# Optimization experiments

Measured on AMD Instinct MI355X. Metric: run time of the kernel, lower is better.

Reference implementation:

```python
import jax, jax.numpy as jnp
import numpy as np

H = 4          # num_heads
MB = 4         # ttt mini_batch_size
GRP = 4        # scan_checkpoint_group_size
TTT_LR = 0.1   # ttt_base_lr
ERF_C = 0.7071067811865476   # 1/sqrt(2)
PDF_C = 0.3989422804014327   # 1/sqrt(2*pi)


def _gelu(z):
    return 0.5 * z * (1.0 + jax.scipy.special.erf(z * ERF_C))


def _gelu_grad(z):
    return 0.5 * (1.0 + jax.scipy.special.erf(z * ERF_C)) + z * jnp.exp(-0.5 * z * z) * PDF_C


def _ln(x, w, b, eps):
    mu = x.mean(-1, keepdims=True)
    var = ((x - mu) ** 2).mean(-1, keepdims=True)
    return w * (x - mu) / jnp.sqrt(var + eps) + b


def _ln_l2_bwd(z, w, b, target, eps=1e-6):
    # grad of 0.5*||LN(z; w, b) - target||^2 w.r.t. z (fused LN backward)
    mu = z.mean(-1, keepdims=True)
    var = ((z - mu) ** 2).mean(-1, keepdims=True)
    std = jnp.sqrt(var + eps)
    zhat = (z - mu) / std
    y = w * zhat + b
    g = w * (y - target)
    return (g - g.mean(-1, keepdims=True) - zhat * (g * zhat).mean(-1, keepdims=True)) / std


def _conv1d(x, w, b, pad):
    # x: [B, Cin, L], w: [Cout, Cin, K]
    y = jax.lax.conv_general_dilated(x, w, (1,), [(pad, pad)], dimension_numbers=("NCH", "OIH", "NCH"))
    return y + b[None, :, None]


def _ttt(x, wq, wk, wv, wo, W1, b1, W2, b2, lnw, lnb):
    # x: [B, L, D];  ttt_mlp fast-weight scan over mini-batches of size MB
    B, L, D = x.shape
    d = D // H
    nmb = L // MB
    ng = nmb // GRP

    def split(w):
        # [B,L,D] -> [ng, GRP, B, H, MB, d]
        return (x @ w).reshape(B, L, H, d).transpose(0, 2, 1, 3).reshape(B, H, ng, GRP, MB, d).transpose(2, 3, 0, 1, 4, 5)

    XQ, XK, XV = split(wq), split(wk), split(wv)
    lw = lnw[None, :, None, :]  # [1,H,1,d]
    lb = lnb[None, :, None, :]
    eta = TTT_LR / MB

    carry = (jnp.broadcast_to(W1, (B, H, d, 4 * d)),
             jnp.broadcast_to(b1, (B, H, 1, 4 * d)),
             jnp.broadcast_to(W2, (B, H, 4 * d, d)),
             jnp.broadcast_to(b2, (B, H, 1, d)))

    def step(c, inp):
        W1c, b1c, W2c, b2c = c
        xq, xk, xv = inp  # each [B,H,MB,d]
        Z1 = jnp.einsum('bhmd,bhdk->bhmk', xk, W1c) + b1c
        X2 = _gelu(Z1)
        Z2 = jnp.einsum('bhmk,bhkd->bhmd', X2, W2c) + b2c
        gZ2 = _ln_l2_bwd(Z2, lw, lb, xv - xk)
        gZ1 = jnp.einsum('bhmd,bhkd->bhmk', gZ2, W2c) * _gelu_grad(Z1)
        W1n = W1c - eta * jnp.einsum('bhmd,bhmk->bhdk', xk, gZ1)
        b1n = b1c - eta * gZ1.sum(2, keepdims=True)
        W2n = W2c - eta * jnp.einsum('bhmk,bhmd->bhkd', X2, gZ2)
        b2n = b2c - eta * gZ2.sum(2, keepdims=True)
        Z1q = jnp.einsum('bhmd,bhdk->bhmk', xq, W1n) + b1n
        Z2q = jnp.einsum('bhmk,bhkd->bhmd', _gelu(Z1q), W2n) + b2n
        return (W1n, b1n, W2n, b2n), xq + _ln(Z2q, lw, lb, 1e-6)

    @jax.checkpoint
    def group(c, inp_g):
        return jax.lax.scan(step, c, inp_g)

    _, out = jax.lax.scan(group, carry, (XQ, XK, XV))  # [ng,GRP,B,H,MB,d]
    out = out.transpose(2, 3, 0, 1, 4, 5).reshape(B, H, L, d).transpose(0, 2, 1, 3).reshape(B, L, D)
    return x + out @ wo


def reference(x, conv1_w, conv1_b, convs_w, convs_b, ln_w, ln_b, wq, wk, wv, wo,
              ttt_W1, ttt_b1, ttt_W2, ttt_b2, ttt_ln_w, ttt_ln_b,
              fc_w, fc_b, fc2_w, fc2_b, fc3_w, fc3_b):
    h = x.transpose(0, 2, 1)                       # [B, dim1, L]
    h = jax.nn.relu(_conv1d(h, conv1_w, conv1_b, 0))
    acts = []
    for i in range(8):
        h = jax.nn.relu(_conv1d(h, convs_w[i], convs_b[i], 1))
        acts.append(h)
    h = acts[1] + acts[3] + acts[5] + acts[7]      # x2 + x4 + x6 + x8
    h = h.transpose(0, 2, 1)                       # [B, L, dim3]
    h = _ln(h, ln_w, ln_b, 1e-5)
    h = _ttt(h, wq, wk, wv, wo, ttt_W1, ttt_b1, ttt_W2, ttt_b2, ttt_ln_w, ttt_ln_b)
    h = _ln(h, ln_w, ln_b, 1e-5)                   # module reuses self.layer_norm
    h = h @ fc_w + fc_b
    h = h @ fc2_w + fc2_b
    return h @ fc3_w + fc3_b                       # [B, L, 1]


def setup_inputs() -> dict:
    key = jax.random.key(0)
    ks = jax.random.split(key, 12)
    B, L, dim1, dim2, dim3 = 4, 1024, 64, 512, 256
    Hn, dh = 4, 64

    def n(k, shape):
        return jax.random.normal(k, shape, jnp.float32) * 0.02

    return {
        "x": jax.random.normal(ks[0], (B, L, dim1), jnp.float32),
        "conv1_w": n(ks[1], (dim3, dim1, 1)),
        "conv1_b": jnp.zeros((dim3,), jnp.float32),
        "convs_w": n(ks[2], (8, dim3, dim3, 3)),
        "convs_b": jnp.zeros((8, dim3), jnp.float32),
        "ln_w": jnp.ones((dim3,), jnp.float32),
        "ln_b": jnp.zeros((dim3,), jnp.float32),
        "wq": n(ks[3], (dim3, dim3)),
        "wk": n(ks[4], (dim3, dim3)),
        "wv": n(ks[5], (dim3, dim3)),
        "wo": n(ks[6], (dim3, dim3)),
        "ttt_W1": n(ks[7], (Hn, dh, 4 * dh)),
        "ttt_b1": jnp.zeros((Hn, 1, 4 * dh), jnp.float32),
        "ttt_W2": n(ks[8], (Hn, 4 * dh, dh)),
        "ttt_b2": jnp.zeros((Hn, 1, dh), jnp.float32),
        "ttt_ln_w": jnp.ones((Hn, dh), jnp.float32),
        "ttt_ln_b": jnp.zeros((Hn, dh), jnp.float32),
        "fc_w": n(ks[9], (dim3, dim2)),
        "fc_b": jnp.zeros((dim2,), jnp.float32),
        "fc2_w": n(ks[10], (dim2, dim1)),
        "fc2_b": jnp.zeros((dim1,), jnp.float32),
        "fc3_w": n(ks[11], (dim1, 1)),
        "fc3_b": jnp.zeros((1,), jnp.float32),
    }
```

## Files before the change

### kernel.cpp

```cpp
#include <hip/hip_runtime.h>
#include <hip/hip_bf16.h>


#define ERF_CF 0.70710678118654752f
#define PDF_CF 0.3989422804014327f
#define ETA 0.025f

typedef __attribute__((ext_vector_type(8))) short bfrag;
typedef __attribute__((ext_vector_type(4))) float f32x4;

union FB { bfrag v; unsigned short u[8]; unsigned d[4]; };

__device__ __forceinline__ float wsum(float v) {
#pragma unroll
  for (int o = 32; o > 0; o >>= 1) v += __shfl_xor(v, o, 64);
  return v;
}

__device__ __forceinline__ unsigned pack_split(float x) {
  unsigned u = __float_as_uint(x);
  unsigned hb = u & 0xFFFF0000u;
  float lf = x - __uint_as_float(hb);
  return hb | (__float_as_uint(lf) >> 16);
}
// ... 52 lines not shown
    val = fc2w[in * 64 + out];
  }
  unsigned short hs, ls;
  split2(val, hs, ls);
  WH[id] = hs;
  WL[id] = ls;
}

__global__ __launch_bounds__(256) void zero_halo_pl(
    unsigned short* __restrict__ cAH, unsigned short* __restrict__ cAL,
    unsigned short* __restrict__ cBH, unsigned short* __restrict__ cBL) {
  int id = blockIdx.x * 256 + threadIdx.x;
  int buf = id >> 11;
  int r = id & 2047;
  int b = r >> 9, row = (r >> 8) & 1, c = r & 255;
  unsigned short* p = buf == 0 ? cAH : buf == 1 ? cAL : buf == 2 ? cBH : cBL;
  p[(b * 1026 + row * 1025) * 256 + c] = 0;
}

template <int AF32, int HALOA, int BIAS, int RELU, int EPI, int ACC>
__global__ __launch_bounds__(256) void gemm_mf(
    const unsigned short* __restrict__ AH, const unsigned short* __restrict__ AL,
    const float* __restrict__ Af32,
    const unsigned short* __restrict__ BH, const unsigned short* __restrict__ BL,
    const float* __restrict__ bias,
    const unsigned short* __restrict__ resH, const unsigned short* __restrict__ resL,
    float* __restrict__ outF, unsigned short* __restrict__ outH,
    unsigned short* __restrict__ outL, float* __restrict__ acc4,
    int N, int K) {
  const int tid = threadIdx.x;
  const int w = tid >> 6, lane = tid & 63;
  const int a = lane & 15, g = lane >> 4;
  const int s = w >> 1, ch = w & 1;
  const int bm = blockIdx.x * 32, bn = blockIdx.y * 64;
  const int rowA = bm + 16 * s + a;
  long abase;
  if constexpr (HALOA)
    abase = (long)((rowA >> 10) * 1026 + (rowA & 1023)) * 256;
  else
    abase = (long)rowA * K;
  const int cb0 = bn + (ch * 2) * 16 + a;
  const int cb1 = cb0 + 16;
  f32x4 acc0 = {0.f, 0.f, 0.f, 0.f}, acc1 = {0.f, 0.f, 0.f, 0.f};
#pragma unroll 2
  for (int kk = 0; kk < K; kk += 32) {
    FB ah, al;
    if constexpr (AF32) {
      const float* ap = Af32 + abase + kk + g * 8;
      float av[8];
      *(float4*)&av[0] = *(const float4*)ap;
      *(float4*)&av[4] = *(const float4*)(ap + 4);
#pragma unroll
      for (int e = 0; e < 8; ++e) split2(av[e], ah.u[e], al.u[e]);
    } else {
      ah.v = *(const bfrag*)&AH[abase + kk + g * 8];
      al.v = *(const bfrag*)&AL[abase + kk + g * 8];
    }
    FB b0h, b0l, b1h, b1l;
    b0h.v = *(const bfrag*)&BH[(long)cb0 * K + kk + g * 8];
    b0l.v = *(const bfrag*)&BL[(long)cb0 * K + kk + g * 8];
    b1h.v = *(const bfrag*)&BH[(long)cb1 * K + kk + g * 8];
    b1l.v = *(const bfrag*)&BL[(long)cb1 * K + kk + g * 8];
    acc0 = mm3(ah.v, al.v, b0h.v, b0l.v, acc0);
    acc1 = mm3(ah.v, al.v, b1h.v, b1l.v, acc1);
  }
#pragma unroll
  for (int i = 0; i < 2; ++i) {
    f32x4 av = i ? acc1 : acc0;
    int col = i ? cb1 : cb0;
    float bv = 0.f;
    if constexpr (BIAS) bv = bias[col];
#pragma unroll
    for (int q = 0; q < 4; ++q) {
      int r = bm + 16 * s + g * 4 + q;
      float val = av[q] + bv;
      if constexpr (RELU) val = fmaxf(val, 0.f);
      if constexpr (EPI == 4) {
        long ri = (long)r * N + col;
        val += uns(resH[ri], resL[ri]);
      }
      if constexpr (EPI == 0 || EPI == 4) {
        outF[(long)r * N + col] = val;
      } else if constexpr (EPI == 1) {
        long hi = (long)((r >> 10) * 1026 + (r & 1023) + 1) * 256 + col;
        unsigned short hs, ls;
        split2(val, hs, ls);
        outH[hi] = hs;
        outL[hi] = ls;
      } else if constexpr (EPI == 2) {
        int b_ = r >> 10, l = r & 1023, hq = col >> 6;
        long oidx = (((long)(b_ * 4 + hq) * 1024 + l) << 6) + (col & 63);
        outF[oidx] = val;
      } else if constexpr (EPI == 3) {
        long oi = (long)r * N + col;
        unsigned short hs, ls;
        split2(val, hs, ls);
        outH[oi] = hs;
        outL[oi] = ls;
      }
      if constexpr (ACC == 1) {
        acc4[(long)r * 256 + col] = val;
      } else if constexpr (ACC == 2) {
        acc4[(long)r * 256 + col] += val;
      }
    }
  }
}

__global__ __launch_bounds__(256) void ln_pl(const float* __restrict__ in,
                                             unsigned short* __restrict__ oH,
                                             unsigned short* __restrict__ oL,
                                             const float* __restrict__ w,
                                             const float* __restrict__ bb,
                                             float eps) {
  int row = blockIdx.x * 4 + (threadIdx.x >> 6);
  int l = threadIdx.x & 63;
  float4 v = ((const float4*)(in + (long)row * 256))[l];
  float s = wsum(v.x + v.y + v.z + v.w);
  float mu = s * (1.0f / 256.0f);
  float dx = v.x - mu, dy = v.y - mu, dz = v.z - mu, dw = v.w - mu;
  float rstd = rsqrtf(wsum(dx * dx + dy * dy + dz * dz + dw * dw) * (1.0f / 256.0f) + eps);
  float4 wv = ((const float4*)w)[l];
  float4 bv = ((const float4*)bb)[l];
  float rr[4];
  rr[0] = wv.x * dx * rstd + bv.x;
  rr[1] = wv.y * dy * rstd + bv.y;
  rr[2] = wv.z * dz * rstd + bv.z;
  rr[3] = wv.w * dw * rstd + bv.w;
  long base = (long)row * 256 + l * 4;
#pragma unroll
  for (int j = 0; j < 4; ++j) {
    unsigned short hs, ls;
    split2(rr[j], hs, ls);
    oH[base + j] = hs;
    oL[base + j] = ls;
  }
}

__global__ __launch_bounds__(512, 2) void ttt_mfma(
    const float* __restrict__ XQ, const float* __restrict__ XK,
    const float* __restrict__ XV, const float* __restrict__ W1i,
    const float* __restrict__ B1i, const float* __restrict__ W2i,
    const float* __restrict__ B2i, const float* __restrict__ LNW,
    const float* __restrict__ LNB, unsigned short* __restrict__ outH,
    unsigned short* __restrict__ outL) {
  extern __shared__ char smem[];
  unsigned short* W2Hp  = (unsigned short*)smem;
  unsigned short* W2Lp  = W2Hp + 256 * 72;
  unsigned short* W2THp = W2Lp + 256 * 72;
  unsigned short* W2TLp = W2THp + 64 * 264;
  unsigned short* X2Hp  = W2TLp + 64 * 264;
  unsigned short* X2Lp  = X2Hp + 4 * 272;
  unsigned short* xkHp  = X2Lp + 4 * 272;
  unsigned short* xkLp  = xkHp + 4 * 80;
  unsigned short* xqHp  = xkLp + 4 * 80;
  unsigned short* xqLp  = xqHp + 4 * 80;
  unsigned short* gZHp  = xqLp + 4 * 80;
  unsigned short* gZLp  = gZHp + 4 * 80;
  float* X2F  = (float*)(gZLp + 4 * 80);
  float* gZ1f = X2F + 4 * 264;
  float* Z2f  = gZ1f + 1024;
  float* redS = Z2f + 256;
  float* xvL  = redS + 512;
  float* b2L  = xvL + 256;
  float* lwL  = b2L + 64;
  float* lbL  = lwL + 64;

  const int bh = blockIdx.x, b = bh >> 2, h = bh & 3;
  const int t = threadIdx.x;
  const int w8 = t >> 6;
  const int lane = t & 63;
  const int a = lane & 15, g = lane >> 4;
  const bool rowv = (a < 4), g0 = (g == 0);
  const int c0 = 32 * w8 + a;
  const int c1 = 32 * w8 + 16 + a;
  const int kh = w8 & 1;
  const int jc = (w8 >> 1) * 16 + a;

  FB zf; zf.d[0] = zf.d[1] = zf.d[2] = zf.d[3] = 0;

  FB w1h[2][2], w1l[2][2];
#pragma unroll
  for (int i = 0; i < 2; ++i) {
    int cc = 32 * w8 + i * 16 + a;
#pragma unroll
    for (int kc = 0; kc < 2; ++kc) {
#pragma unroll
      for (int e = 0; e < 8; ++e) {
        int k = kc * 32 + g * 8 + e;
        unsigned p = pack_split(W1i[(h * 64 + k) * 256 + cc]);
        w1h[i][kc].u[e] = (unsigned short)(p >> 16);
        w1l[i][kc].u[e] = (unsigned short)(p & 0xFFFFu);
      }
    }
  }
  float b1r0 = B1i[h * 256 + c0];
  float b1r1 = B1i[h * 256 + c1];

  for (int i = 0; i < 32; ++i) {
    int id = t + i * 512;
    int k = id >> 6, j = id & 63;
    unsigned p = pack_split(W2i[(h * 256 + k) * 64 + j]);
    W2Hp[k * 72 + j] = (unsigned short)(p >> 16);
    W2Lp[k * 72 + j] = (unsigned short)(p & 0xFFFFu);
    int j2 = id >> 8, k2 = id & 255;
    unsigned q = pack_split(W2i[(h * 256 + k2) * 64 + j2]);
    W2THp[j2 * 264 + k2] = (unsigned short)(q >> 16);
    W2TLp[j2 * 264 + k2] = (unsigned short)(q & 0xFFFFu);
  }
  if (t < 64) { b2L[t] = B2i[h * 64 + t]; lwL[t] = LNW[h * 64 + t]; lbL[t] = LNB[h * 64 + t]; }

  const long chain = (long)bh * 65536;
  float rk = 0.f, rv = 0.f, rq = 0.f;
  if (t >= 256) {
    int u = t - 256;
    rk = XK[chain + u]; rv = XV[chain + u]; rq = XQ[chain + u];
  }

  for (int n = 0; n < 256; ++n) {
    if (t >= 256) {
      int u = t - 256, m = u >> 6, k = u & 63;
      unsigned short hs, ls;
      split2(rk, hs, ls); xkHp[m * 80 + k] = hs; xkLp[m * 80 + k] = ls;
      split2(rq, hs, ls); xqHp[m * 80 + k] = hs; xqLp[m * 80 + k] = ls;
      xvL[u] = rv;
    }
    __syncthreads();

    float gpA[4] = {0.f, 0.f, 0.f, 0.f}, gpB[4] = {0.f, 0.f, 0.f, 0.f};

    {
      f32x4 A0 = (f32x4){b1r0, b1r0, b1r0, b1r0};
      f32x4 A1 = (f32x4){b1r1, b1r1, b1r1, b1r1};
#pragma unroll
      for (int kc = 0; kc < 2; ++kc) {
        int base = kc * 32 + g * 8;
        FB ah = zf, al = zf;
        if (rowv) {
          ah.v = *(const bfrag*)&xkHp[a * 80 + base];
          al.v = *(const bfrag*)&xkLp[a * 80 + base];
        }
        A0 = mm3(ah.v, al.v, w1h[0][kc].v, w1l[0][kc].v, A0);
        A1 = mm3(ah.v, al.v, w1h[1][kc].v, w1l[1][kc].v, A1);
      }
      if (g0) {
#pragma unroll
        for (int q = 0; q < 4; ++q) {
          float z = A0[q];
          float er = erff(z * ERF_CF);
          float hh = 0.5f * (1.0f + er);
          float x2 = z * hh;
          gpA[q] = hh + z * __expf(-0.5f * z * z) * PDF_CF;
          unsigned short hs, ls;
          split2(x2, hs, ls);
          X2Hp[q * 272 + c0] = hs; X2Lp[q * 272 + c0] = ls;
          X2F[q * 264 + c0] = x2;
          z = A1[q];
          er = erff(z * ERF_CF);
          hh = 0.5f * (1.0f + er);
          x2 = z * hh;
          gpB[q] = hh + z * __expf(-0.5f * z * z) * PDF_CF;
          split2(x2, hs, ls);
          X2Hp[q * 272 + c1] = hs; X2Lp[q * 272 + c1] = ls;
          X2F[q * 264 + c1] = x2;
        }
      }
    }
    __syncthreads();

    {
      f32x4 acc = (f32x4){0.f, 0.f, 0.f, 0.f};
#pragma unroll
      for (int k4 = 0; k4 < 4; ++k4) {
        int base = (kh * 4 + k4) * 32 + g * 8;
        FB ah = zf, al = zf, bhf, blf;
        if (rowv) {
          ah.v = *(const bfrag*)&X2Hp[a * 272 + base];
          al.v = *(const bfrag*)&X2Lp[a * 272 + base];
        }
        bhf.v = *(const bfrag*)&W2THp[jc * 264 + base];
        blf.v = *(const bfrag*)&W2TLp[jc * 264 + base];
        acc = mm3(ah.v, al.v, bhf.v, blf.v, acc);
      }
      if (g0) {
#pragma unroll
        for (int q = 0; q < 4; ++q) redS[(kh * 4 + q) * 64 + jc] = acc[q];
      }
    }
    __syncthreads();

    if (t < 256) {
      int m = w8, j = lane;
      float z2 = b2L[j] + redS[m * 64 + j] + redS[256 + m * 64 + j];
      float mu = wsum(z2) * (1.0f / 64.0f);
      float dv = z2 - mu;
      float var = wsum(dv * dv) * (1.0f / 64.0f);
      float stdv = sqrtf(var + 1e-6f);
      float zh = dv / stdv;
      float lw = lwL[j], lb = lbL[j];
      float xkf = uns(xkHp[m * 80 + j], xkLp[m * 80 + j]);
      float tgt = xvL[m * 64 + j] - xkf;
      float gg = lw * (lw * zh + lb - tgt);
      float gs = wsum(gg) * (1.0f / 64.0f);
      float gzs = wsum(gg * zh) * (1.0f / 64.0f);
      float gz2 = (gg - gs - zh * gzs) / stdv;
      unsigned short hs, ls;
      split2(gz2, hs, ls);
      gZHp[m * 80 + j] = hs; gZLp[m * 80 + j] = ls;
      Z2f[m * 64 + j] = gz2;
    } else if (n + 1 < 256) {
      int u = t - 256;
      long nb = chain + (long)(n + 1) * 256;
      rk = XK[nb + u]; rv = XV[nb + u]; rq = XQ[nb + u];
    }
    __syncthreads();

    {
      f32x4 A0 = (f32x4){0.f, 0.f, 0.f, 0.f};
      f32x4 A1 = (f32x4){0.f, 0.f, 0.f, 0.f};
#pragma unroll
      for (int kc = 0; kc < 2; ++kc) {
        int base = kc * 32 + g * 8;
        FB ah = zf, al = zf, b0h, b0l, b1h, b1l;
        if (rowv) {
          ah.v = *(const bfrag*)&gZHp[a * 80 + base];
          al.v = *(const bfrag*)&gZLp[a * 80 + base];
        }
        b0h.v = *(const bfrag*)&W2Hp[c0 * 72 + base];
        b0l.v = *(const bfrag*)&W2Lp[c0 * 72 + base];
        b1h.v = *(const bfrag*)&W2Hp[c1 * 72 + base];
        b1l.v = *(const bfrag*)&W2Lp[c1 * 72 + base];
        A0 = mm3(ah.v, al.v, b0h.v, b0l.v, A0);
        A1 = mm3(ah.v, al.v, b1h.v, b1l.v, A1);
      }
      if (g0) {
#pragma unroll
        for (int q = 0; q < 4; ++q) {
          gZ1f[q * 256 + c0] = A0[q] * gpA[q];
          gZ1f[q * 256 + c1] = A1[q] * gpB[q];
        }
      }
      {
        int jr = t & 63, kb = (t >> 6) * 32;
        float gz0 = Z2f[jr], gz1 = Z2f[64 + jr], gz2 = Z2f[128 + jr], gz3 = Z2f[192 + jr];
#pragma unroll
        for (int kk = 0; kk < 32; kk += 8) {
          int kb8 = kb + kk;
          float x0[8], x1[8], x2[8], x3[8];
          *(float4*)&x0[0] = *(const float4*)&X2F[kb8];        *(float4*)&x0[4] = *(const float4*)&X2F[kb8 + 4];
          *(float4*)&x1[0] = *(const float4*)&X2F[264 + kb8];  *(float4*)&x1[4] = *(const float4*)&X2F[264 + kb8 + 4];
          *(float4*)&x2[0] = *(const float4*)&X2F[528 + kb8];  *(float4*)&x2[4] = *(const float4*)&X2F[528 + kb8 + 4];
          *(float4*)&x3[0] = *(const float4*)&X2F[792 + kb8];  *(float4*)&x3[4] = *(const float4*)&X2F[792 + kb8 + 4];
          FB oh, ol, nh, nl;
          oh.v = *(const bfrag*)&W2THp[jr * 264 + kb8];
          ol.v = *(const bfrag*)&W2TLp[jr * 264 + kb8];
#pragma unroll
          for (int e = 0; e < 8; ++e) {
            float uu = fmaf(x3[e], gz3, fmaf(x2[e], gz2, fmaf(x1[e], gz1, x0[e] * gz0)));
            float f = fmaf(-ETA, uu, fb_el(oh, ol, e));
            unsigned short hs, ls;
            split2(f, hs, ls);
            nh.u[e] = hs; nl.u[e] = ls;
          }
          *(bfrag*)&W2THp[jr * 264 + kb8] = nh.v;
          *(bfrag*)&W2TLp[jr * 264 + kb8] = nl.v;
        }
      }
    }
    __syncthreads();

    {
      float gzA0 = gZ1f[c0], gzA1 = gZ1f[256 + c0], gzA2 = gZ1f[512 + c0], gzA3 = gZ1f[768 + c0];
      float gzB0 = gZ1f[c1], gzB1 = gZ1f[256 + c1], gzB2 = gZ1f[512 + c1], gzB3 = gZ1f[768 + c1];
      b1r0 = fmaf(-ETA, ((gzA0 + gzA1) + gzA2) + gzA3, b1r0);
      b1r1 = fmaf(-ETA, ((gzB0 + gzB1) + gzB2) + gzB3, b1r1);
#pragma unroll
      for (int kc = 0; kc < 2; ++kc) {
        int base = kc * 32 + g * 8;
        FB x0h, x0l, x1h, x1l, x2h, x2l, x3h, x3l;
        x0h.v = *(const bfrag*)&xkHp[base];       x0l.v = *(const bfrag*)&xkLp[base];
        x1h.v = *(const bfrag*)&xkHp[80 + base];  x1l.v = *(const bfrag*)&xkLp[80 + base];
        x2h.v = *(const bfrag*)&xkHp[160 + base]; x2l.v = *(const bfrag*)&xkLp[160 + base];
        x3h.v = *(const bfrag*)&xkHp[240 + base]; x3l.v = *(const bfrag*)&xkLp[240 + base];
#pragma unroll
        for (int e = 0; e < 8; ++e) {
          float k0 = fb_el(x0h, x0l, e), k1 = fb_el(x1h, x1l, e);
          float k2 = fb_el(x2h, x2l, e), k3 = fb_el(x3h, x3l, e);
          float uA = fmaf(k3, gzA3, fmaf(k2, gzA2, fmaf(k1, gzA1, k0 * gzA0)));
          float uB = fmaf(k3, gzB3, fmaf(k2, gzB2, fmaf(k1, gzB1, k0 * gzB0)));
          float fA = fmaf(-ETA, uA, fb_el(w1h[0][kc], w1l[0][kc], e));
          float fB = fmaf(-ETA, uB, fb_el(w1h[1][kc], w1l[1][kc], e));
          unsigned short hs, ls;
          split2(fA, hs, ls); w1h[0][kc].u[e] = hs; w1l[0][kc].u[e] = ls;
          split2(fB, hs, ls); w1h[1][kc].u[e] = hs; w1l[1][kc].u[e] = ls;
        }
      }
      {
        f32x4 A0 = (f32x4){b1r0, b1r0, b1r0, b1r0};
        f32x4 A1 = (f32x4){b1r1, b1r1, b1r1, b1r1};
#pragma unroll
        for (int kc = 0; kc < 2; ++kc) {
          int base = kc * 32 + g * 8;
          FB ah = zf, al = zf;
          if (rowv) {
            ah.v = *(const bfrag*)&xqHp[a * 80 + base];
            al.v = *(const bfrag*)&xqLp[a * 80 + base];
          }
          A0 = mm3(ah.v, al.v, w1h[0][kc].v, w1l[0][kc].v, A0);
          A1 = mm3(ah.v, al.v, w1h[1][kc].v, w1l[1][kc].v, A1);
        }
        if (g0) {
#pragma unroll
          for (int q = 0; q < 4; ++q) {
            float z = A0[q];
            float x2 = 0.5f * z * (1.0f + erff(z * ERF_CF));
            unsigned short hs, ls;
            split2(x2, hs, ls);
            X2Hp[q * 272 + c0] = hs; X2Lp[q * 272 + c0] = ls;
            z = A1[q];
            x2 = 0.5f * z * (1.0f + erff(z * ERF_CF));
            split2(x2, hs, ls);
            X2Hp[q * 272 + c1] = hs; X2Lp[q * 272 + c1] = ls;
          }
        }
      }
      {
        int kr = t & 255, jh = (t >> 8) * 32;
        float xk0 = X2F[kr], xk1 = X2F[264 + kr], xk2 = X2F[528 + kr], xk3 = X2F[792 + kr];
#pragma unroll
        for (int jj = 0; jj < 32; jj += 8) {
          int jb = jh + jj;
          float g0f[8], g1f[8], g2f[8], g3f[8];
          *(float4*)&g0f[0] = *(const float4*)&Z2f[jb];        *(float4*)&g0f[4] = *(const float4*)&Z2f[jb + 4];
          *(float4*)&g1f[0] = *(const float4*)&Z2f[64 + jb];   *(float4*)&g1f[4] = *(const float4*)&Z2f[64 + jb + 4];
          *(float4*)&g2f[0] = *(const float4*)&Z2f[128 + jb];  *(float4*)&g2f[4] = *(const float4*)&Z2f[128 + jb + 4];
          *(float4*)&g3f[0] = *(const float4*)&Z2f[192 + jb];  *(float4*)&g3f[4] = *(const float4*)&Z2f[192 + jb + 4];
          FB oh, ol, nh, nl;
          oh.v = *(const bfrag*)&W2Hp[kr * 72 + jb];
          ol.v = *(const bfrag*)&W2Lp[kr * 72 + jb];
#pragma unroll
          for (int e = 0; e < 8; ++e) {
            float uu = fmaf(xk3, g3f[e], fmaf(xk2, g2f[e], fmaf(xk1, g1f[e], xk0 * g0f[e])));
            float f = fmaf(-ETA, uu, fb_el(oh, ol, e));
            unsigned short hs, ls;
            split2(f, hs, ls);
            nh.u[e] = hs; nl.u[e] = ls;
          }
          *(bfrag*)&W2Hp[kr * 72 + jb] = nh.v;
          *(bfrag*)&W2Lp[kr * 72 + jb] = nl.v;
        }
      }
      if (t < 64)
        b2L[t] -= ETA * (((Z2f[t] + Z2f[64 + t]) + Z2f[128 + t]) + Z2f[192 + t]);
    }
    __syncthreads();

    {
      f32x4 acc = (f32x4){0.f, 0.f, 0.f, 0.f};
#pragma unroll
      for (int k4 = 0; k4 < 4; ++k4) {
        int base = (kh * 4 + k4) * 32 + g * 8;
        FB ah = zf, al = zf, bhf, blf;
        if (rowv) {
          ah.v = *(const bfrag*)&X2Hp[a * 272 + base];
          al.v = *(const bfrag*)&X2Lp[a * 272 + base];
        }
        bhf.v = *(const bfrag*)&W2THp[jc * 264 + base];
        blf.v = *(const bfrag*)&W2TLp[jc * 264 + base];
        acc = mm3(ah.v, al.v, bhf.v, blf.v, acc);
      }
      if (g0) {
#pragma unroll
        for (int q = 0; q < 4; ++q) redS[(kh * 4 + q) * 64 + jc] = acc[q];
      }
    }
    __syncthreads();

    if (t < 256) {
      int m = w8, j = lane;
      float z = b2L[j] + redS[m * 64 + j] + redS[256 + m * 64 + j];
      float mu = wsum(z) * (1.0f / 64.0f);
      float dv = z - mu;
      float var = wsum(dv * dv) * (1.0f / 64.0f);
      float rstd = rsqrtf(var + 1e-6f);
      float xqf = uns(xqHp[m * 80 + j], xqLp[m * 80 + j]);
      float val = lwL[j] * dv * rstd + lbL[j] + xqf;
      long oidx = ((long)(b * 1024 + n * 4 + m)) * 256 + h * 64 + j;
      unsigned short hs, ls;
      split2(val, hs, ls);
      outH[oidx] = hs;
      outL[oidx] = ls;
    }
    __syncthreads();
  }
}

__global__ __launch_bounds__(256) void fc3_kernel(const float* __restrict__ f2,
                                                  const float* __restrict__ w,
                                                  const float* __restrict__ bias,
                                                  float* __restrict__ o) {
  int m = blockIdx.x * 4 + (threadIdx.x >> 6);
  int lane = threadIdx.x & 63;
  float v = f2[m * 64 + lane] * w[lane];
  v = wsum(v);
  if (lane == 0) o[m] = v + bias[0];
}

extern "C" void kernel_launch(void* const* d_in, const int* in_sizes, int n_in,
                              void* d_out, int out_size, void* d_ws, size_t ws_size,
                              hipStream_t stream) {
  const float* x       = (const float*)d_in[0];
  const float* conv1_w = (const float*)d_in[1];
  const float* conv1_b = (const float*)d_in[2];
  const float* convs_w = (const float*)d_in[3];
  const float* convs_b = (const float*)d_in[4];
  const float* ln_w    = (const float*)d_in[5];
  const float* ln_b    = (const float*)d_in[6];
  const float* wq      = (const float*)d_in[7];
  const float* wk      = (const float*)d_in[8];
  const float* wv      = (const float*)d_in[9];
  const float* wo      = (const float*)d_in[10];
  const float* ttt_W1  = (const float*)d_in[11];
  const float* ttt_b1  = (const float*)d_in[12];
  const float* ttt_W2  = (const float*)d_in[13];
  const float* ttt_b2  = (const float*)d_in[14];
  const float* ttt_lnw = (const float*)d_in[15];
  const float* ttt_lnb = (const float*)d_in[16];
  const float* fc_w    = (const float*)d_in[17];
  const float* fc_b    = (const float*)d_in[18];
  const float* fc2_w   = (const float*)d_in[19];
  const float* fc2_b   = (const float*)d_in[20];
  const float* fc3_w   = (const float*)d_in[21];
  const float* fc3_b   = (const float*)d_in[22];

  unsigned short* U = (unsigned short*)d_ws;
  unsigned short* WH   = U;
  unsigned short* WL   = U + 2015232;
  unsigned short* cAH  = U + 4030464;
  unsigned short* cAL  = U + 5081088;
  unsigned short* cBH  = U + 6131712;
  unsigned short* cBL  = U + 7182336;
  unsigned short* tlnH = U + 8232960;
  unsigned short* tlnL = U + 9281536;
  unsigned short* toH  = U + 10330112;
  unsigned short* toL  = U + 11378688;
  float* F = (float*)d_ws;
  float* sum4 = F + 6213632;
  float* XQ   = sum4;
  float* tfull = sum4;
  float* XK   = F + 7262208;
  float* XV   = F + 8310784;
  unsigned short* f1H = (unsigned short*)XK;
  unsigned short* f1L = (unsigned short*)XV;
  float* f2 = (float*)toH;
  unsigned short* h2H = cAH;
  unsigned short* h2L = cAL;

  const int W_WT1 = 0, W_WT = 16384, W_QKVO = 1589248, W_FC = 1851392, W_FC2 = 1982464;

  dim3 blk(256);

  zero_halo_pl<<<32, blk, 0, stream>>>(cAH, cAL, cBH, cBL);
  prep_all<<<7872, blk, 0, stream>>>(conv1_w, convs_w, wq, wk, wv, wo, fc_w,
                                     fc2_w, WH, WL);

  gemm_mf<1, 0, 1, 1, 1, 0><<<dim3(128, 4), blk, 0, stream>>>(
      nullptr, nullptr, x, WH + W_WT1, WL + W_WT1, conv1_b, nullptr, nullptr,
      nullptr, cAH, cAL, nullptr, 256, 64);

  for (int i = 0; i < 8; ++i) {
    const unsigned short* iH = (i % 2 == 0) ? cAH : cBH;
    const unsigned short* iL = (i % 2 == 0) ? cAL : cBL;
    unsigned short* oH = (i % 2 == 0) ? cBH : cAH;
    unsigned short* oL = (i % 2 == 0) ? cBL : cAL;
    const unsigned short* bH = WH + W_WT + i * 196608;
    const unsigned short* bL = WL + W_WT + i * 196608;
    const float* bp = convs_b + i * 256;
    if (i == 1)
      gemm_mf<0, 1, 1, 1, 1, 1><<<dim3(128, 4), blk, 0, stream>>>(
          iH, iL, nullptr, bH, bL, bp, nullptr, nullptr, nullptr, oH, oL, sum4,
          256, 768);
    else if (i == 3 || i == 5 || i == 7)
      gemm_mf<0, 1, 1, 1, 1, 2><<<dim3(128, 4), blk, 0, stream>>>(
          iH, iL, nullptr, bH, bL, bp, nullptr, nullptr, nullptr, oH, oL, sum4,
          256, 768);
    else
      gemm_mf<0, 1, 1, 1, 1, 0><<<dim3(128, 4), blk, 0, stream>>>(
          iH, iL, nullptr, bH, bL, bp, nullptr, nullptr, nullptr, oH, oL,
          nullptr, 256, 768);
  }

  ln_pl<<<1024, blk, 0, stream>>>(sum4, tlnH, tlnL, ln_w, ln_b, 1e-5f);

  gemm_mf<0, 0, 0, 0, 2, 0><<<dim3(128, 4), blk, 0, stream>>>(
      tlnH, tlnL, nullptr, WH + W_QKVO + 0 * 65536, WL + W_QKVO + 0 * 65536,
      nullptr, nullptr, nullptr, XQ, nullptr, nullptr, nullptr, 256, 256);
  gemm_mf<0, 0, 0, 0, 2, 0><<<dim3(128, 4), blk, 0, stream>>>(
      tlnH, tlnL, nullptr, WH + W_QKVO + 1 * 65536, WL + W_QKVO + 1 * 65536,
      nullptr, nullptr, nullptr, XK, nullptr, nullptr, nullptr, 256, 256);
  gemm_mf<0, 0, 0, 0, 2, 0><<<dim3(128, 4), blk, 0, stream>>>(
      tlnH, tlnL, nullptr, WH + W_QKVO + 2 * 65536, WL + W_QKVO + 2 * 65536,
      nullptr, nullptr, nullptr, XV, nullptr, nullptr, nullptr, 256, 256);

  const int TTT_LDS = 162688;
  (void)hipFuncSetAttribute((const void*)ttt_mfma,
                            hipFuncAttributeMaxDynamicSharedMemorySize, TTT_LDS);
  ttt_mfma<<<16, dim3(512), TTT_LDS, stream>>>(XQ, XK, XV, ttt_W1, ttt_b1,
                                               ttt_W2, ttt_b2, ttt_lnw, ttt_lnb,
                                               toH, toL);

  gemm_mf<0, 0, 0, 0, 4, 0><<<dim3(128, 4), blk, 0, stream>>>(
      toH, toL, nullptr, WH + W_QKVO + 3 * 65536, WL + W_QKVO + 3 * 65536,
      nullptr, tlnH, tlnL, tfull, nullptr, nullptr, nullptr, 256, 256);

  ln_pl<<<1024, blk, 0, stream>>>(tfull, h2H, h2L, ln_w, ln_b, 1e-5f);

  gemm_mf<0, 0, 1, 0, 3, 0><<<dim3(128, 8), blk, 0, stream>>>(
      h2H, h2L, nullptr, WH + W_FC, WL + W_FC, fc_b, nullptr, nullptr, nullptr,
      f1H, f1L, nullptr, 512, 256);
  gemm_mf<0, 0, 1, 0, 0, 0><<<dim3(128, 1), blk, 0, stream>>>(
      f1H, f1L, nullptr, WH + W_FC2, WL + W_FC2, fc2_b, nullptr, nullptr, f2,
      nullptr, nullptr, nullptr, 64, 512);
  fc3_kernel<<<1024, blk, 0, stream>>>(f2, fc3_w, fc3_b, (float*)d_out);
}
```

Before: 2.931 ms.

## Compute TTT query outputs with Gram-matrix correction instead of post-update matmuls

Before the weights are updated, the query projection through the old W1 is computed together with the key projection. The post-update Z1 and Z2 for the queries are then built algebraically from Gram terms (xq·xk and X2q·X2k) and the gradients. This removes the dependence of the output stage on the updated W1 and W2 and cuts one barrier per mini-batch from the sequential scan. The cost is extra MFMA work, extra shuffle reductions, and possible numeric differences from reassociating the terms.

```diff
diff --git a/kernel.cpp b/kernel.cpp
--- a/kernel.cpp
+++ b/kernel.cpp
@@ -241,6 +241,8 @@
   float* b2L  = xvL + 256;
   float* lwL  = b2L + 64;
   float* lbL  = lwL + 64;
+  float* G1L  = lbL + 64;
+  float* G2L  = G1L + 16;
 
   const int bh = blockIdx.x, b = bh >> 2, h = bh & 3;
   const int t = threadIdx.x;
@@ -252,6 +254,9 @@
   const int c1 = 32 * w8 + 16 + a;
   const int kh = w8 & 1;
   const int jc = (w8 >> 1) * 16 + a;
+  const int gp_ = 2 * w8 + (lane >> 5);
+  const int gmq = gp_ >> 2, gmk = gp_ & 3;
+  const int gr = lane & 31;
 
   FB zf; zf.d[0] = zf.d[1] = zf.d[2] = zf.d[3] = 0;
 
@@ -308,16 +313,22 @@
     {
       f32x4 A0 = (f32x4){b1r0, b1r0, b1r0, b1r0};
       f32x4 A1 = (f32x4){b1r1, b1r1, b1r1, b1r1};
+      f32x4 Q0 = (f32x4){b1r0, b1r0, b1r0, b1r0};
+      f32x4 Q1 = (f32x4){b1r1, b1r1, b1r1, b1r1};
 #pragma unroll
       for (int kc = 0; kc < 2; ++kc) {
         int base = kc * 32 + g * 8;
-        FB ah = zf, al = zf;
+        FB kh_ = zf, kl_ = zf, qh_ = zf, ql_ = zf;
         if (rowv) {
-          ah.v = *(const bfrag*)&xkHp[a * 80 + base];
-          al.v = *(const bfrag*)&xkLp[a * 80 + base];
-        }
-        A0 = mm3(ah.v, al.v, w1h[0][kc].v, w1l[0][kc].v, A0);
-        A1 = mm3(ah.v, al.v, w1h[1][kc].v, w1l[1][kc].v, A1);
+          kh_.v = *(const bfrag*)&xkHp[a * 80 + base];
+          kl_.v = *(const bfrag*)&xkLp[a * 80 + base];
+          qh_.v = *(const bfrag*)&xqHp[a * 80 + base];
+          ql_.v = *(const bfrag*)&xqLp[a * 80 + base];
+        }
+        A0 = mm3(kh_.v, kl_.v, w1h[0][kc].v, w1l[0][kc].v, A0);
+        A1 = mm3(kh_.v, kl_.v, w1h[1][kc].v, w1l[1][kc].v, A1);
+        Q0 = mm3(qh_.v, ql_.v, w1h[0][kc].v, w1l[0][kc].v, Q0);
+        Q1 = mm3(qh_.v, ql_.v, w1h[1][kc].v, w1l[1][kc].v, Q1);
       }
       if (g0) {
 #pragma unroll
@@ -339,6 +350,8 @@
           split2(x2, hs, ls);
           X2Hp[q * 272 + c1] = hs; X2Lp[q * 272 + c1] = ls;
           X2F[q * 264 + c1] = x2;
+          gZ1f[q * 256 + c0] = Q0[q];
+          gZ1f[q * 256 + c1] = Q1[q];
         }
       }
     }
@@ -362,6 +375,16 @@
 #pragma unroll
         for (int q = 0; q < 4; ++q) redS[(kh * 4 + q) * 64 + jc] = acc[q];
       }
+      float s = uns(xqHp[gmq * 80 + gr], xqLp[gmq * 80 + gr]) *
+                    uns(xkHp[gmk * 80 + gr], xkLp[gmk * 80 + gr]) +
+                uns(xqHp[gmq * 80 + gr + 32], xqLp[gmq * 80 + gr + 32]) *
+                    uns(xkHp[gmk * 80 + gr + 32], xkLp[gmk * 80 + gr + 32]);
+      s += __shfl_xor(s, 16, 64);
+      s += __shfl_xor(s, 8, 64);
+      s += __shfl_xor(s, 4, 64);
+      s += __shfl_xor(s, 2, 64);
+      s += __shfl_xor(s, 1, 64);
+      if (gr == 0) G1L[gp_] = s;
     }
     __syncthreads();
 
@@ -410,12 +433,144 @@
         A1 = mm3(ah.v, al.v, b1h.v, b1l.v, A1);
       }
       if (g0) {
+        float gzc0[4], gzc1[4], q0v[4], q1v[4];
 #pragma unroll
         for (int q = 0; q < 4; ++q) {
-          gZ1f[q * 256 + c0] = A0[q] * gpA[q];
-          gZ1f[q * 256 + c1] = A1[q] * gpB[q];
-        }
-      }
+          gzc0[q] = A0[q] * gpA[q];
+          gzc1[q] = A1[q] * gpB[q];
+          q0v[q] = gZ1f[q * 256 + c0];
+          q1v[q] = gZ1f[q * 256 + c1];
+        }
+#pragma unroll
+        for (int q = 0; q < 4; ++q) {
+          float d0 = G1L[q * 4 + 0] + 1.0f, d1 = G1L[q * 4 + 1] + 1.0f;
+          float d2 = G1L[q * 4 + 2] + 1.0f, d3 = G1L[q * 4 + 3] + 1.0f;
+          float corr0 = fmaf(d3, gzc0[3], fmaf(d2, gzc0[2], fmaf(d1, gzc0[1], d0 * gzc0[0])));
+          float corr1 = fmaf(d3, gzc1[3], fmaf(d2, gzc1[2], fmaf(d1, gzc1[1], d0 * gzc1[0])));
+          float z0 = fmaf(-ETA, corr0, q0v[q]);
+          float z1 = fmaf(-ETA, corr1, q1v[q]);
+          float x20 = 0.5f * z0 * (1.0f + erff(z0 * ERF_CF));
+          float x21 = 0.5f * z1 * (1.0f + erff(z1 * ERF_CF));
+          unsigned short hs, ls;
+          split2(x20, hs, ls);
+          X2Hp[q * 272 + c0] = hs; X2Lp[q * 272 + c0] = ls;
+          split2(x21, hs, ls);
+          X2Hp[q * 272 + c1] = hs; X2Lp[q * 272 + c1] = ls;
+          gZ1f[q * 256 + c0] = gzc0[q];
+          gZ1f[q * 256 + c1] = gzc1[q];
+        }
+      }
+    }
+    __syncthreads();
+
+    float b2r = 0.f;
+    {
+      f32x4 acc = (f32x4){0.f, 0.f, 0.f, 0.f};
+#pragma unroll
+      for (int k4 = 0; k4 < 4; ++k4) {
+        int base = (kh * 4 + k4) * 32 + g * 8;
+        FB ah = zf, al = zf, bhf, blf;
+        if (rowv) {
+          ah.v = *(const bfrag*)&X2Hp[a * 272 + base];
+          al.v = *(const bfrag*)&X2Lp[a * 272 + base];
+        }
+        bhf.v = *(const bfrag*)&W2THp[jc * 264 + base];
+        blf.v = *(const bfrag*)&W2TLp[jc * 264 + base];
+        acc = mm3(ah.v, al.v, bhf.v, blf.v, acc);
+      }
+      if (g0) {
+#pragma unroll
+        for (int q = 0; q < 4; ++q) redS[(kh * 4 + q) * 64 + jc] = acc[q];
+      }
+      float s = 0.f;
+#pragma unroll
+      for (int kk = 0; kk < 256; kk += 32)
+        s = fmaf(uns(X2Hp[gmq * 272 + kk + gr], X2Lp[gmq * 272 + kk + gr]),
+                 X2F[gmk * 264 + kk + gr], s);
+      s += __shfl_xor(s, 16, 64);
+      s += __shfl_xor(s, 8, 64);
+      s += __shfl_xor(s, 4, 64);
+      s += __shfl_xor(s, 2, 64);
+      s += __shfl_xor(s, 1, 64);
+      if (gr == 0) G2L[gp_] = s;
+      float gzA0 = gZ1f[c0], gzA1 = gZ1f[256 + c0], gzA2 = gZ1f[512 + c0], gzA3 = gZ1f[768 + c0];
+      float gzB0 = gZ1f[c1], gzB1 = gZ1f[256 + c1], gzB2 = gZ1f[512 + c1], gzB3 = gZ1f[768 + c1];
+      b1r0 = fmaf(-ETA, ((gzA0 + gzA1) + gzA2) + gzA3, b1r0);
+      b1r1 = fmaf(-ETA, ((gzB0 + gzB1) + gzB2) + gzB3, b1r1);
+#pragma unroll
+      for (int kc = 0; kc < 2; ++kc) {
+        int base = kc * 32 + g * 8;
+        FB x0h, x0l, x1h, x1l, x2h, x2l, x3h, x3l;
+        x0h.v = *(const bfrag*)&xkHp[base];       x0l.v = *(const bfrag*)&xkLp[base];
+        x1h.v = *(const bfrag*)&xkHp[80 + base];  x1l.v = *(const bfrag*)&xkLp[80 + base];
+        x2h.v = *(const bfrag*)&xkHp[160 + base]; x2l.v = *(const bfrag*)&xkLp[160 + base];
+        x3h.v = *(const bfrag*)&xkHp[240 + base]; x3l.v = *(const bfrag*)&xkLp[240 + base];
+#pragma unroll
+        for (int e = 0; e < 8; ++e) {
+          float k0 = fb_el(x0h, x0l, e), k1 = fb_el(x1h, x1l, e);
+          float k2 = fb_el(x2h, x2l, e), k3 = fb_el(x3h, x3l, e);
+          float uA = fmaf(k3, gzA3, fmaf(k2, gzA2, fmaf(k1, gzA1, k0 * gzA0)));
+          float uB = fmaf(k3, gzB3, fmaf(k2, gzB2, fmaf(k1, gzB1, k0 * gzB0)));
+          float fA = fmaf(-ETA, uA, fb_el(w1h[0][kc], w1l[0][kc], e));
+          float fB = fmaf(-ETA, uB, fb_el(w1h[1][kc], w1l[1][kc], e));
+          unsigned short hs, ls;
+          split2(fA, hs, ls); w1h[0][kc].u[e] = hs; w1l[0][kc].u[e] = ls;
+          split2(fB, hs, ls); w1h[1][kc].u[e] = hs; w1l[1][kc].u[e] = ls;
+        }
+      }
+      {
+        int kr = t & 255, jh = (t >> 8) * 32;
+        float xk0 = X2F[kr], xk1 = X2F[264 + kr], xk2 = X2F[528 + kr], xk3 = X2F[792 + kr];
+#pragma unroll
+        for (int jj = 0; jj < 32; jj += 8) {
+          int jb = jh + jj;
+          float g0f[8], g1f[8], g2f[8], g3f[8];
+          *(float4*)&g0f[0] = *(const float4*)&Z2f[jb];        *(float4*)&g0f[4] = *(const float4*)&Z2f[jb + 4];
+          *(float4*)&g1f[0] = *(const float4*)&Z2f[64 + jb];   *(float4*)&g1f[4] = *(const float4*)&Z2f[64 + jb + 4];
+          *(float4*)&g2f[0] = *(const float4*)&Z2f[128 + jb];  *(float4*)&g2f[4] = *(const float4*)&Z2f[128 + jb + 4];
+          *(float4*)&g3f[0] = *(const float4*)&Z2f[192 + jb];  *(float4*)&g3f[4] = *(const float4*)&Z2f[192 + jb + 4];
+          FB oh, ol, nh, nl;
+          oh.v = *(const bfrag*)&W2Hp[kr * 72 + jb];
+          ol.v = *(const bfrag*)&W2Lp[kr * 72 + jb];
+#pragma unroll
+          for (int e = 0; e < 8; ++e) {
+            float uu = fmaf(xk3, g3f[e], fmaf(xk2, g2f[e], fmaf(xk1, g1f[e], xk0 * g0f[e])));
+            float f = fmaf(-ETA, uu, fb_el(oh, ol, e));
+            unsigned short hs, ls;
+            split2(f, hs, ls);
+            nh.u[e] = hs; nl.u[e] = ls;
+          }
+          *(bfrag*)&W2Hp[kr * 72 + jb] = nh.v;
+          *(bfrag*)&W2Lp[kr * 72 + jb] = nl.v;
+        }
+      }
+      if (t < 256) b2r = b2L[lane];
+    }
+    __syncthreads();
+
+    {
+      if (t < 256) {
+        int m = w8, j = lane;
+        float z = b2r + redS[m * 64 + j] + redS[256 + m * 64 + j];
+        float corr = fmaf(G2L[m * 4 + 0] + 1.f, Z2f[j],
+                     fmaf(G2L[m * 4 + 1] + 1.f, Z2f[64 + j],
+                     fmaf(G2L[m * 4 + 2] + 1.f, Z2f[128 + j],
+                          (G2L[m * 4 + 3] + 1.f) * Z2f[192 + j])));
+        z = fmaf(-ETA, corr, z);
+        float mu = wsum(z) * (1.0f / 64.0f);
+        float dv = z - mu;
+        float var = wsum(dv * dv) * (1.0f / 64.0f);
+        float rstd = rsqrtf(var + 1e-6f);
+        float xqf = uns(xqHp[m * 80 + j], xqLp[m * 80 + j]);
+        float val = lwL[j] * dv * rstd + lbL[j] + xqf;
+        long oidx = ((long)(b * 1024 + n * 4 + m)) * 256 + h * 64 + j;
+        unsigned short hs, ls;
+        split2(val, hs, ls);
+        outH[oidx] = hs;
+        outL[oidx] = ls;
+      }
+      if (t < 64)
+        b2L[t] -= ETA * (((Z2f[t] + Z2f[64 + t]) + Z2f[128 + t]) + Z2f[192 + t]);
       {
         int jr = t & 63, kb = (t >> 6) * 32;
         float gz0 = Z2f[jr], gz1 = Z2f[64 + jr], gz2 = Z2f[128 + jr], gz3 = Z2f[192 + jr];
@@ -442,130 +597,6 @@
           *(bfrag*)&W2TLp[jr * 264 + kb8] = nl.v;
         }
       }
-    }
-    __syncthreads();
-
-    {
-      float gzA0 = gZ1f[c0], gzA1 = gZ1f[256 + c0], gzA2 = gZ1f[512 + c0], gzA3 = gZ1f[768 + c0];
-      float gzB0 = gZ1f[c1], gzB1 = gZ1f[256 + c1], gzB2 = gZ1f[512 + c1], gzB3 = gZ1f[768 + c1];
-      b1r0 = fmaf(-ETA, ((gzA0 + gzA1) + gzA2) + gzA3, b1r0);
-      b1r1 = fmaf(-ETA, ((gzB0 + gzB1) + gzB2) + gzB3, b1r1);
-#pragma unroll
-      for (int kc = 0; kc < 2; ++kc) {
-        int base = kc * 32 + g * 8;
-        FB x0h, x0l, x1h, x1l, x2h, x2l, x3h, x3l;
-        x0h.v = *(const bfrag*)&xkHp[base];       x0l.v = *(const bfrag*)&xkLp[base];
-        x1h.v = *(const bfrag*)&xkHp[80 + base];  x1l.v = *(const bfrag*)&xkLp[80 + base];
-        x2h.v = *(const bfrag*)&xkHp[160 + base]; x2l.v = *(const bfrag*)&xkLp[160 + base];
-        x3h.v = *(const bfrag*)&xkHp[240 + base]; x3l.v = *(const bfrag*)&xkLp[240 + base];
-#pragma unroll
-        for (int e = 0; e < 8; ++e) {
-          float k0 = fb_el(x0h, x0l, e), k1 = fb_el(x1h, x1l, e);
-          float k2 = fb_el(x2h, x2l, e), k3 = fb_el(x3h, x3l, e);
-          float uA = fmaf(k3, gzA3, fmaf(k2, gzA2, fmaf(k1, gzA1, k0 * gzA0)));
-          float uB = fmaf(k3, gzB3, fmaf(k2, gzB2, fmaf(k1, gzB1, k0 * gzB0)));
-          float fA = fmaf(-ETA, uA, fb_el(w1h[0][kc], w1l[0][kc], e));
-          float fB = fmaf(-ETA, uB, fb_el(w1h[1][kc], w1l[1][kc], e));
-          unsigned short hs, ls;
-          split2(fA, hs, ls); w1h[0][kc].u[e] = hs; w1l[0][kc].u[e] = ls;
-          split2(fB, hs, ls); w1h[1][kc].u[e] = hs; w1l[1][kc].u[e] = ls;
-        }
-      }
-      {
-        f32x4 A0 = (f32x4){b1r0, b1r0, b1r0, b1r0};
-        f32x4 A1 = (f32x4){b1r1, b1r1, b1r1, b1r1};
-#pragma unroll
-        for (int kc = 0; kc < 2; ++kc) {
-          int base = kc * 32 + g * 8;
-          FB ah = zf, al = zf;
-          if (rowv) {
-            ah.v = *(const bfrag*)&xqHp[a * 80 + base];
-            al.v = *(const bfrag*)&xqLp[a * 80 + base];
-          }
-          A0 = mm3(ah.v, al.v, w1h[0][kc].v, w1l[0][kc].v, A0);
-          A1 = mm3(ah.v, al.v, w1h[1][kc].v, w1l[1][kc].v, A1);
-        }
-        if (g0) {
-#pragma unroll
-          for (int q = 0; q < 4; ++q) {
-            float z = A0[q];
-            float x2 = 0.5f * z * (1.0f + erff(z * ERF_CF));
-            unsigned short hs, ls;
-            split2(x2, hs, ls);
-            X2Hp[q * 272 + c0] = hs; X2Lp[q * 272 + c0] = ls;
-            z = A1[q];
-            x2 = 0.5f * z * (1.0f + erff(z * ERF_CF));
-            split2(x2, hs, ls);
-            X2Hp[q * 272 + c1] = hs; X2Lp[q * 272 + c1] = ls;
-          }
-        }
-      }
-      {
-        int kr = t & 255, jh = (t >> 8) * 32;
-        float xk0 = X2F[kr], xk1 = X2F[264 + kr], xk2 = X2F[528 + kr], xk3 = X2F[792 + kr];
-#pragma unroll
-        for (int jj = 0; jj < 32; jj += 8) {
-          int jb = jh + jj;
-          float g0f[8], g1f[8], g2f[8], g3f[8];
-          *(float4*)&g0f[0] = *(const float4*)&Z2f[jb];        *(float4*)&g0f[4] = *(const float4*)&Z2f[jb + 4];
-          *(float4*)&g1f[0] = *(const float4*)&Z2f[64 + jb];   *(float4*)&g1f[4] = *(const float4*)&Z2f[64 + jb + 4];
-          *(float4*)&g2f[0] = *(const float4*)&Z2f[128 + jb];  *(float4*)&g2f[4] = *(const float4*)&Z2f[128 + jb + 4];
-          *(float4*)&g3f[0] = *(const float4*)&Z2f[192 + jb];  *(float4*)&g3f[4] = *(const float4*)&Z2f[192 + jb + 4];
-          FB oh, ol, nh, nl;
-          oh.v = *(const bfrag*)&W2Hp[kr * 72 + jb];
-          ol.v = *(const bfrag*)&W2Lp[kr * 72 + jb];
-#pragma unroll
-          for (int e = 0; e < 8; ++e) {
-            float uu = fmaf(xk3, g3f[e], fmaf(xk2, g2f[e], fmaf(xk1, g1f[e], xk0 * g0f[e])));
-            float f = fmaf(-ETA, uu, fb_el(oh, ol, e));
-            unsigned short hs, ls;
-            split2(f, hs, ls);
-            nh.u[e] = hs; nl.u[e] = ls;
-          }
-          *(bfrag*)&W2Hp[kr * 72 + jb] = nh.v;
-          *(bfrag*)&W2Lp[kr * 72 + jb] = nl.v;
-        }
-      }
-      if (t < 64)
-        b2L[t] -= ETA * (((Z2f[t] + Z2f[64 + t]) + Z2f[128 + t]) + Z2f[192 + t]);
-    }
-    __syncthreads();
-
-    {
-      f32x4 acc = (f32x4){0.f, 0.f, 0.f, 0.f};
-#pragma unroll
-      for (int k4 = 0; k4 < 4; ++k4) {
-        int base = (kh * 4 + k4) * 32 + g * 8;
-        FB ah = zf, al = zf, bhf, blf;
-        if (rowv) {
-          ah.v = *(const bfrag*)&X2Hp[a * 272 + base];
-          al.v = *(const bfrag*)&X2Lp[a * 272 + base];
-        }
-        bhf.v = *(const bfrag*)&W2THp[jc * 264 + base];
-        blf.v = *(const bfrag*)&W2TLp[jc * 264 + base];
-        acc = mm3(ah.v, al.v, bhf.v, blf.v, acc);
-      }
-      if (g0) {
-#pragma unroll
-        for (int q = 0; q < 4; ++q) redS[(kh * 4 + q) * 64 + jc] = acc[q];
-      }
-    }
-    __syncthreads();
-
-    if (t < 256) {
-      int m = w8, j = lane;
-      float z = b2L[j] + redS[m * 64 + j] + redS[256 + m * 64 + j];
-      float mu = wsum(z) * (1.0f / 64.0f);
-      float dv = z - mu;
-      float var = wsum(dv * dv) * (1.0f / 64.0f);
-      float rstd = rsqrtf(var + 1e-6f);
-      float xqf = uns(xqHp[m * 80 + j], xqLp[m * 80 + j]);
-      float val = lwL[j] * dv * rstd + lbL[j] + xqf;
-      long oidx = ((long)(b * 1024 + n * 4 + m)) * 256 + h * 64 + j;
-      unsigned short hs, ls;
-      split2(val, hs, ls);
-      outH[oidx] = hs;
-      outL[oidx] = ls;
     }
     __syncthreads();
   }
@@ -678,7 +709,7 @@
       tlnH, tlnL, nullptr, WH + W_QKVO + 2 * 65536, WL + W_QKVO + 2 * 65536,
       nullptr, nullptr, nullptr, XV, nullptr, nullptr, nullptr, 256, 256);
 
-  const int TTT_LDS = 162688;
+  const int TTT_LDS = 162816;
   (void)hipFuncSetAttribute((const void*)ttt_mfma,
                             hipFuncAttributeMaxDynamicSharedMemorySize, TTT_LDS);
   ttt_mfma<<<16, dim3(512), TTT_LDS, stream>>>(XQ, XK, XV, ttt_W1, ttt_b1,
```

Result: slower. 3.368 ms (+14.9%).

## Remove per-step barrier in TTT scan by staging next inputs early, double-buffering xq

Applied to the files above, without the earlier changes.

The idle upper threads now write the next mini-batch's split xk/xq/xv into shared memory during the final output stage of the current step, so the barrier at the top of each of the 256 scan iterations can be dropped. xq is double-buffered because the current step's output still reads it while the next one is being written. Row padding shrinks from 80 to 72 elements, and s_setprio is raised around the MFMA loops to favour matrix issue. The risk is races on xk/xv if any later read of them falls after the final stage, and the 72-element stride may change LDS bank conflicts.

```diff
diff --git a/kernel.cpp b/kernel.cpp
--- a/kernel.cpp
+++ b/kernel.cpp
@@ -228,12 +228,12 @@
   unsigned short* X2Hp  = W2TLp + 64 * 264;
   unsigned short* X2Lp  = X2Hp + 4 * 272;
   unsigned short* xkHp  = X2Lp + 4 * 272;
-  unsigned short* xkLp  = xkHp + 4 * 80;
-  unsigned short* xqHp  = xkLp + 4 * 80;
-  unsigned short* xqLp  = xqHp + 4 * 80;
-  unsigned short* gZHp  = xqLp + 4 * 80;
-  unsigned short* gZLp  = gZHp + 4 * 80;
-  float* X2F  = (float*)(gZLp + 4 * 80);
+  unsigned short* xkLp  = xkHp + 4 * 72;
+  unsigned short* xqHp  = xkLp + 4 * 72;
+  unsigned short* xqLp  = xqHp + 2 * 4 * 72;
+  unsigned short* gZHp  = xqLp + 2 * 4 * 72;
+  unsigned short* gZLp  = gZHp + 4 * 72;
+  float* X2F  = (float*)(gZLp + 4 * 72);
   float* gZ1f = X2F + 4 * 264;
   float* Z2f  = gZ1f + 1024;
   float* redS = Z2f + 256;
@@ -289,36 +289,35 @@
   const long chain = (long)bh * 65536;
   float rk = 0.f, rv = 0.f, rq = 0.f;
   if (t >= 256) {
-    int u = t - 256;
+    int u = t - 256, m = u >> 6, k = u & 63;
     rk = XK[chain + u]; rv = XV[chain + u]; rq = XQ[chain + u];
-  }
+    unsigned short hs, ls;
+    split2(rk, hs, ls); xkHp[m * 72 + k] = hs; xkLp[m * 72 + k] = ls;
+    split2(rq, hs, ls); xqHp[m * 72 + k] = hs; xqLp[m * 72 + k] = ls;
+    xvL[u] = rv;
+  }
+  __syncthreads();
 
   for (int n = 0; n < 256; ++n) {
-    if (t >= 256) {
-      int u = t - 256, m = u >> 6, k = u & 63;
-      unsigned short hs, ls;
-      split2(rk, hs, ls); xkHp[m * 80 + k] = hs; xkLp[m * 80 + k] = ls;
-      split2(rq, hs, ls); xqHp[m * 80 + k] = hs; xqLp[m * 80 + k] = ls;
-      xvL[u] = rv;
-    }
-    __syncthreads();
-
+    const int XQO = (n & 1) * 288;
     float gpA[4] = {0.f, 0.f, 0.f, 0.f}, gpB[4] = {0.f, 0.f, 0.f, 0.f};
 
     {
       f32x4 A0 = (f32x4){b1r0, b1r0, b1r0, b1r0};
       f32x4 A1 = (f32x4){b1r1, b1r1, b1r1, b1r1};
+      __builtin_amdgcn_s_setprio(1);
 #pragma unroll
       for (int kc = 0; kc < 2; ++kc) {
         int base = kc * 32 + g * 8;
         FB ah = zf, al = zf;
         if (rowv) {
-          ah.v = *(const bfrag*)&xkHp[a * 80 + base];
-          al.v = *(const bfrag*)&xkLp[a * 80 + base];
+          ah.v = *(const bfrag*)&xkHp[a * 72 + base];
+          al.v = *(const bfrag*)&xkLp[a * 72 + base];
         }
         A0 = mm3(ah.v, al.v, w1h[0][kc].v, w1l[0][kc].v, A0);
         A1 = mm3(ah.v, al.v, w1h[1][kc].v, w1l[1][kc].v, A1);
       }
+      __builtin_amdgcn_s_setprio(0);
       if (g0) {
 #pragma unroll
         for (int q = 0; q < 4; ++q) {
@@ -346,6 +345,7 @@
 
     {
       f32x4 acc = (f32x4){0.f, 0.f, 0.f, 0.f};
+      __builtin_amdgcn_s_setprio(1);
 #pragma unroll
       for (int k4 = 0; k4 < 4; ++k4) {
         int base = (kh * 4 + k4) * 32 + g * 8;
@@ -358,6 +358,7 @@
         blf.v = *(const bfrag*)&W2TLp[jc * 264 + base];
         acc = mm3(ah.v, al.v, bhf.v, blf.v, acc);
       }
+      __builtin_amdgcn_s_setprio(0);
       if (g0) {
 #pragma unroll
         for (int q = 0; q < 4; ++q) redS[(kh * 4 + q) * 64 + jc] = acc[q];
@@ -374,7 +375,7 @@
       float stdv = sqrtf(var + 1e-6f);
       float zh = dv / stdv;
       float lw = lwL[j], lb = lbL[j];
-      float xkf = uns(xkHp[m * 80 + j], xkLp[m * 80 + j]);
+      float xkf = uns(xkHp[m * 72 + j], xkLp[m * 72 + j]);
       float tgt = xvL[m * 64 + j] - xkf;
       float gg = lw * (lw * zh + lb - tgt);
       float gs = wsum(gg) * (1.0f / 64.0f);
@@ -382,7 +383,7 @@
       float gz2 = (gg - gs - zh * gzs) / stdv;
       unsigned short hs, ls;
       split2(gz2, hs, ls);
-      gZHp[m * 80 + j] = hs; gZLp[m * 80 + j] = ls;
+      gZHp[m * 72 + j] = hs; gZLp[m * 72 + j] = ls;
       Z2f[m * 64 + j] = gz2;
     } else if (n + 1 < 256) {
       int u = t - 256;
@@ -394,13 +395,14 @@
     {
       f32x4 A0 = (f32x4){0.f, 0.f, 0.f, 0.f};
       f32x4 A1 = (f32x4){0.f, 0.f, 0.f, 0.f};
+      __builtin_amdgcn_s_setprio(1);
 #pragma unroll
       for (int kc = 0; kc < 2; ++kc) {
         int base = kc * 32 + g * 8;
         FB ah = zf, al = zf, b0h, b0l, b1h, b1l;
         if (rowv) {
-          ah.v = *(const bfrag*)&gZHp[a * 80 + base];
-          al.v = *(const bfrag*)&gZLp[a * 80 + base];
+          ah.v = *(const bfrag*)&gZHp[a * 72 + base];
+          al.v = *(const bfrag*)&gZLp[a * 72 + base];
         }
         b0h.v = *(const bfrag*)&W2Hp[c0 * 72 + base];
         b0l.v = *(const bfrag*)&W2Lp[c0 * 72 + base];
@@ -409,6 +411,7 @@
         A0 = mm3(ah.v, al.v, b0h.v, b0l.v, A0);
         A1 = mm3(ah.v, al.v, b1h.v, b1l.v, A1);
       }
+      __builtin_amdgcn_s_setprio(0);
       if (g0) {
 #pragma unroll
         for (int q = 0; q < 4; ++q) {
@@ -455,9 +458,9 @@
         int base = kc * 32 + g * 8;
         FB x0h, x0l, x1h, x1l, x2h, x2l, x3h, x3l;
         x0h.v = *(const bfrag*)&xkHp[base];       x0l.v = *(const bfrag*)&xkLp[base];
-        x1h.v = *(const bfrag*)&xkHp[80 + base];  x1l.v = *(const bfrag*)&xkLp[80 + base];
-        x2h.v = *(const bfrag*)&xkHp[160 + base]; x2l.v = *(const bfrag*)&xkLp[160 + base];
-        x3h.v = *(const bfrag*)&xkHp[240 + base]; x3l.v = *(const bfrag*)&xkLp[240 + base];
+        x1h.v = *(const bfrag*)&xkHp[72 + base];  x1l.v = *(const bfrag*)&xkLp[72 + base];
+        x2h.v = *(const bfrag*)&xkHp[144 + base]; x2l.v = *(const bfrag*)&xkLp[144 + base];
+        x3h.v = *(const bfrag*)&xkHp[216 + base]; x3l.v = *(const bfrag*)&xkLp[216 + base];
 #pragma unroll
         for (int e = 0; e < 8; ++e) {
           float k0 = fb_el(x0h, x0l, e), k1 = fb_el(x1h, x1l, e);
@@ -474,17 +477,19 @@
       {
         f32x4 A0 = (f32x4){b1r0, b1r0, b1r0, b1r0};
         f32x4 A1 = (f32x4){b1r1, b1r1, b1r1, b1r1};
+        __builtin_amdgcn_s_setprio(1);
 #pragma unroll
         for (int kc = 0; kc < 2; ++kc) {
           int base = kc * 32 + g * 8;
           FB ah = zf, al = zf;
           if (rowv) {
-            ah.v = *(const bfrag*)&xqHp[a * 80 + base];
-            al.v = *(const bfrag*)&xqLp[a * 80 + base];
+            ah.v = *(const bfrag*)&xqHp[XQO + a * 72 + base];
+            al.v = *(const bfrag*)&xqLp[XQO + a * 72 + base];
           }
           A0 = mm3(ah.v, al.v, w1h[0][kc].v, w1l[0][kc].v, A0);
           A1 = mm3(ah.v, al.v, w1h[1][kc].v, w1l[1][kc].v, A1);
         }
+        __builtin_amdgcn_s_setprio(0);
         if (g0) {
 #pragma unroll
           for (int q = 0; q < 4; ++q) {
@@ -533,6 +538,7 @@
 
     {
       f32x4 acc = (f32x4){0.f, 0.f, 0.f, 0.f};
+      __builtin_amdgcn_s_setprio(1);
 #pragma unroll
       for (int k4 = 0; k4 < 4; ++k4) {
         int base = (kh * 4 + k4) * 32 + g * 8;
@@ -545,6 +551,7 @@
         blf.v = *(const bfrag*)&W2TLp[jc * 264 + base];
         acc = mm3(ah.v, al.v, bhf.v, blf.v, acc);
       }
+      __builtin_amdgcn_s_setprio(0);
       if (g0) {
 #pragma unroll
         for (int q = 0; q < 4; ++q) redS[(kh * 4 + q) * 64 + jc] = acc[q];
@@ -559,13 +566,20 @@
       float dv = z - mu;
       float var = wsum(dv * dv) * (1.0f / 64.0f);
       float rstd = rsqrtf(var + 1e-6f);
-      float xqf = uns(xqHp[m * 80 + j], xqLp[m * 80 + j]);
+      float xqf = uns(xqHp[XQO + m * 72 + j], xqLp[XQO + m * 72 + j]);
       float val = lwL[j] * dv * rstd + lbL[j] + xqf;
       long oidx = ((long)(b * 1024 + n * 4 + m)) * 256 + h * 64 + j;
       unsigned short hs, ls;
       split2(val, hs, ls);
       outH[oidx] = hs;
       outL[oidx] = ls;
+    } else if (n + 1 < 256) {
+      int u = t - 256, m = u >> 6, k = u & 63;
+      int XQN = ((n + 1) & 1) * 288;
+      unsigned short hs, ls;
+      split2(rk, hs, ls); xkHp[m * 72 + k] = hs; xkLp[m * 72 + k] = ls;
+      split2(rq, hs, ls); xqHp[XQN + m * 72 + k] = hs; xqLp[XQN + m * 72 + k] = ls;
+      xvL[u] = rv;
     }
     __syncthreads();
   }
@@ -678,7 +692,7 @@
       tlnH, tlnL, nullptr, WH + W_QKVO + 2 * 65536, WL + W_QKVO + 2 * 65536,
       nullptr, nullptr, nullptr, XV, nullptr, nullptr, nullptr, 256, 256);
 
-  const int TTT_LDS = 162688;
+  const int TTT_LDS = 163456;
   (void)hipFuncSetAttribute((const void*)ttt_mfma,
                             hipFuncAttributeMaxDynamicSharedMemorySize, TTT_LDS);
   ttt_mfma<<<16, dim3(512), TTT_LDS, stream>>>(XQ, XK, XV, ttt_W1, ttt_b1,
```

Result: no change. 2.876 ms (-1.9%).
